# Kernel optimization log

Hardware: AMD Instinct MI355X
Metric: run time of the kernel (lower is better)

Reference implementation:

```python
import jax, jax.numpy as jnp
import numpy as np
from jax import lax

SEQ_LEN = 8192
TAGS = 2048

def setup_inputs() -> dict:
    key = jax.random.key(0)
    k1, k2, k3, k4, k5 = jax.random.split(key, 5)
    feats = jax.random.normal(k1, (SEQ_LEN, TAGS), dtype=jnp.float32)
    tags = jax.random.randint(k2, (SEQ_LEN,), 0, TAGS, dtype=jnp.int32)
    # nn.Parameter(torch.rand(...)) -> uniform [0,1)
    transitions = jax.random.uniform(k3, (TAGS, TAGS), dtype=jnp.float32)
    transitions_start = jax.random.uniform(k4, (TAGS,), dtype=jnp.float32)
    transitions_stop = jax.random.uniform(k5, (TAGS,), dtype=jnp.float32)
    return {
        "feats": feats,
        "transitions": transitions,
        "transitions_start": transitions_start,
        "transitions_stop": transitions_stop,
        "tags": tags,
    }

def reference(feats, transitions, transitions_start, transitions_stop, tags):
    # Linear-chain CRF negative log-likelihood.
    # transitions[next, prev] = score of transitioning prev -> next.
    L = feats.shape[0]

    # ---- forward (partition) score via log-sum-exp recurrence ----
    fv0 = transitions_start + feats[0]  # [T]

    def step(fv, feat):
        # new[j] = logsumexp_i(fv[i] + transitions[j, i]) + feat[j]
        nfv = jax.nn.logsumexp(fv[None, :] + transitions, axis=1) + feat
        return nfv, None

    fv, _ = lax.scan(step, fv0, feats[1:])
    forward_score = jax.nn.logsumexp(fv + transitions_stop)

    # ---- gold path score ----
    gold = (
        transitions_start[tags[0]]
        + feats[0, tags[0]]
        + jnp.sum(transitions[tags[1:], tags[:-1]])
        + jnp.sum(feats[jnp.arange(1, L), tags[1:]])
        + transitions_stop[tags[-1]]
    )

    return forward_score - gold
```

## Files before the change

### kernel.cpp

```cpp
#include <hip/hip_runtime.h>

#define SEQ  8192
#define NT   2048
#define NBLK 256
#define NTHR 512
#define LOG2E 1.4426950408889634f
#define LN2   0.6931471805599453f

#define LOAD_AG(p)     __hip_atomic_load((p), __ATOMIC_RELAXED, __HIP_MEMORY_SCOPE_AGENT)
#define STORE_AG(p, v) __hip_atomic_store((p), (v), __ATOMIC_RELAXED, __HIP_MEMORY_SCOPE_AGENT)

__device__ unsigned int g_z[2][NT];
__device__ float g_gold;

__device__ __forceinline__ unsigned int f32_to_bf16(float f) {
    unsigned int u = __float_as_uint(f);
    return (u + 0x7FFFu + ((u >> 16) & 1u)) >> 16;
}

__global__ void crf_init(const float* __restrict__ feats,
                         const float* __restrict__ tstart) {
    int i = blockIdx.x * blockDim.x + threadIdx.x;
    if (i < NT) {
        float z0 = __builtin_exp2f((tstart[i] + feats[i]) * LOG2E);
        g_z[0][i] = f32_to_bf16(z0);
        g_z[1][i] = 0xFFFF0000u;
    }
}

__global__ void crf_gold(const float* __restrict__ feats,
                         const float* __restrict__ trans,
                         const float* __restrict__ tstart,
                         const float* __restrict__ tstop,
                         const int*   __restrict__ tags) {
    __shared__ float part[16];
    int tid = threadIdx.x;
    float acc = 0.f;
    for (int t = 1 + tid; t < SEQ; t += 1024) {
        int cur = tags[t], prev = tags[t - 1];
        acc += trans[(size_t)cur * NT + prev] + feats[(size_t)t * NT + cur];
    }
    #pragma unroll
    for (int m = 1; m < 64; m <<= 1) acc += __shfl_xor(acc, m, 64);
    if ((tid & 63) == 0) part[tid >> 6] = acc;
    __syncthreads();
    if (tid == 0) {
        float S = 0.f;
        #pragma unroll
        for (int w = 0; w < 16; ++w) S += part[w];
        int t0 = tags[0], tl = tags[SEQ - 1];
        g_gold = S + tstart[t0] + feats[t0] + tstop[tl];
    }
}

__global__ void __launch_bounds__(NTHR)
crf_main(const float* __restrict__ feats, const float* __restrict__ trans,
         const float* __restrict__ tstop, float* __restrict__ out) {
    const int b   = blockIdx.x;
    const int tid = threadIdx.x;
    const int wv  = tid >> 6;
    const int l   = tid & 63;
    const int j   = b * 8 + wv;

    __shared__ float w_lds[2][NT];
    __shared__ float s_scale[2];
    __shared__ float red[8];

    float E[32];
    {
        const float* trow = trans + (size_t)j * NT;
        #pragma unroll
        for (int k = 0; k < 32; ++k)
            E[k] = __builtin_exp2f(trow[l + (k << 6)] * LOG2E);
    }

    float featv = feats[(size_t)NT + j];
    int esum = 0;

    for (int t = 1; t < SEQ; ++t) {
        const int par = (t - 1) & 1;
        const unsigned int need = (unsigned int)(t - 1);
        unsigned int* buf = g_z[par];

        #pragma unroll
        for (int q = 0; q < 4; ++q) {
            int i = tid + q * NTHR;
            unsigned int v;
            do { v = LOAD_AG(&buf[i]); } while ((v >> 16) != need);
            w_lds[par][i] = __uint_as_float(v << 16);
        }
        if (tid == 0) {
            unsigned int bits = __float_as_uint(w_lds[par][0]);
            int e = (int)((bits >> 23) & 0xFFu) - 127;
            s_scale[par] = __uint_as_float((unsigned int)(127 - e) << 23);
            esum += e;
        }
        float featnext = (t + 1 < SEQ) ? feats[(size_t)(t + 1) * NT + j] : 0.f;
        __syncthreads();

        float acc = 0.f;
        #pragma unroll
        for (int k = 0; k < 32; ++k)
            acc = fmaf(E[k], w_lds[par][l + (k << 6)], acc);
        #pragma unroll
        for (int m = 1; m < 64; m <<= 1) acc += __shfl_xor(acc, m, 64);

        if (l == 0) {
            float znew = acc * s_scale[par] * __builtin_exp2f(featv * LOG2E);
            STORE_AG(&g_z[t & 1][j],
                     ((unsigned int)t << 16) | f32_to_bf16(znew));
        }
        featv = featnext;
    }

    if (b == 0) {
        const unsigned int need = SEQ - 1;
        unsigned int* buf = g_z[(SEQ - 1) & 1];
        float acc = 0.f;
        #pragma unroll
        for (int q = 0; q < 4; ++q) {
            int i = tid + q * NTHR;
            unsigned int v;
            do { v = LOAD_AG(&buf[i]); } while ((v >> 16) != need);
            float w = __uint_as_float(v << 16);
            acc += w * __builtin_exp2f(tstop[i] * LOG2E);
        }
        #pragma unroll
        for (int m = 1; m < 64; m <<= 1) acc += __shfl_xor(acc, m, 64);
        if (l == 0) red[wv] = acc;
        __syncthreads();
        if (tid == 0) {
            float S = 0.f;
            #pragma unroll
            for (int w = 0; w < 8; ++w) S += red[w];
            float fwd = (__builtin_log2f(S) + (float)esum) * LN2;
            out[0] = fwd - g_gold;
        }
    }
}

extern "C" void kernel_launch(void* const* d_in, const int* in_sizes, int n_in,
                              void* d_out, int out_size, void* d_ws, size_t ws_size,
                              hipStream_t stream) {
    const float* feats  = (const float*)d_in[0];
    const float* trans  = (const float*)d_in[1];
    const float* tstart = (const float*)d_in[2];
    const float* tstop  = (const float*)d_in[3];
    const int*   tags   = (const int*)d_in[4];
    float* out = (float*)d_out;

    hipLaunchKernelGGL(crf_init, dim3(2), dim3(1024), 0, stream, feats, tstart);
    hipLaunchKernelGGL(crf_gold, dim3(1), dim3(1024), 0, stream,
                       feats, trans, tstart, tstop, tags);
    hipLaunchKernelGGL(crf_main, dim3(NBLK), dim3(NTHR), 0, stream,
                       feats, trans, tstop, out);
}
```

Before: 22.30 ms.

## Poll z vector with 64-bit atomic loads using 128 blocks of 1024 threads

Halves the number of persistent blocks and doubles the threads per block, so each thread polls a single 64-bit word holding two tagged bf16 values instead of four separate 32-bit words. This cuts per-step polling loads and the number of blocks contending on the global handoff each step. The exp of the next feature value is also computed ahead of the barrier. In exchange, 1024-thread blocks with 32 register-resident exp(transition) values per thread may raise register pressure, and each block's barrier now covers twice as many waves.

```diff
diff --git a/kernel.cpp b/kernel.cpp
--- a/kernel.cpp
+++ b/kernel.cpp
@@ -2,15 +2,15 @@
 
 #define SEQ  8192
 #define NT   2048
-#define NBLK 256
-#define NTHR 512
+#define NBLK 128
+#define NTHR 1024
 #define LOG2E 1.4426950408889634f
 #define LN2   0.6931471805599453f
 
-#define LOAD_AG(p)     __hip_atomic_load((p), __ATOMIC_RELAXED, __HIP_MEMORY_SCOPE_AGENT)
+#define LOAD_AG64(p)   __hip_atomic_load((p), __ATOMIC_RELAXED, __HIP_MEMORY_SCOPE_AGENT)
 #define STORE_AG(p, v) __hip_atomic_store((p), (v), __ATOMIC_RELAXED, __HIP_MEMORY_SCOPE_AGENT)
 
-__device__ unsigned int g_z[2][NT];
+__device__ __align__(16) unsigned int g_z[2][NT];
 __device__ float g_gold;
 
 __device__ __forceinline__ unsigned int f32_to_bf16(float f) {
@@ -60,11 +60,11 @@
     const int tid = threadIdx.x;
     const int wv  = tid >> 6;
     const int l   = tid & 63;
-    const int j   = b * 8 + wv;
+    const int j   = b * 16 + wv;
 
     __shared__ float w_lds[2][NT];
     __shared__ float s_scale[2];
-    __shared__ float red[8];
+    __shared__ float red[16];
 
     float E[32];
     {
@@ -74,28 +74,30 @@
             E[k] = __builtin_exp2f(trow[l + (k << 6)] * LOG2E);
     }
 
-    float featv = feats[(size_t)NT + j];
+    float fexp = __builtin_exp2f(feats[(size_t)NT + j] * LOG2E);
     int esum = 0;
 
     for (int t = 1; t < SEQ; ++t) {
         const int par = (t - 1) & 1;
         const unsigned int need = (unsigned int)(t - 1);
-        unsigned int* buf = g_z[par];
+        unsigned long long* buf64 = (unsigned long long*)g_z[par];
 
-        #pragma unroll
-        for (int q = 0; q < 4; ++q) {
-            int i = tid + q * NTHR;
-            unsigned int v;
-            do { v = LOAD_AG(&buf[i]); } while ((v >> 16) != need);
-            w_lds[par][i] = __uint_as_float(v << 16);
-        }
+        const unsigned long long want =
+            ((unsigned long long)need << 48) | ((unsigned long long)need << 16);
+        unsigned long long v;
+        do { v = LOAD_AG64(&buf64[tid]); }
+        while ((v & 0xFFFF0000FFFF0000ull) != want);
+
+        w_lds[par][2 * tid]     = __uint_as_float((unsigned int)(v & 0xFFFFu) << 16);
+        w_lds[par][2 * tid + 1] = __uint_as_float((unsigned int)((v >> 32) & 0xFFFFu) << 16);
+
         if (tid == 0) {
-            unsigned int bits = __float_as_uint(w_lds[par][0]);
-            int e = (int)((bits >> 23) & 0xFFu) - 127;
+            int e = (int)(((v >> 7) & 0xFFu)) - 127;
             s_scale[par] = __uint_as_float((unsigned int)(127 - e) << 23);
             esum += e;
         }
-        float featnext = (t + 1 < SEQ) ? feats[(size_t)(t + 1) * NT + j] : 0.f;
+        float fexpnext = (t + 1 < SEQ)
+            ? __builtin_exp2f(feats[(size_t)(t + 1) * NT + j] * LOG2E) : 0.f;
         __syncthreads();
 
         float acc = 0.f;
@@ -106,25 +108,26 @@
         for (int m = 1; m < 64; m <<= 1) acc += __shfl_xor(acc, m, 64);
 
         if (l == 0) {
-            float znew = acc * s_scale[par] * __builtin_exp2f(featv * LOG2E);
+            float znew = acc * s_scale[par] * fexp;
             STORE_AG(&g_z[t & 1][j],
                      ((unsigned int)t << 16) | f32_to_bf16(znew));
         }
-        featv = featnext;
+        fexp = fexpnext;
     }
 
     if (b == 0) {
         const unsigned int need = SEQ - 1;
-        unsigned int* buf = g_z[(SEQ - 1) & 1];
-        float acc = 0.f;
-        #pragma unroll
-        for (int q = 0; q < 4; ++q) {
-            int i = tid + q * NTHR;
-            unsigned int v;
-            do { v = LOAD_AG(&buf[i]); } while ((v >> 16) != need);
-            float w = __uint_as_float(v << 16);
-            acc += w * __builtin_exp2f(tstop[i] * LOG2E);
-        }
+        unsigned long long* buf64 = (unsigned long long*)g_z[(SEQ - 1) & 1];
+        const unsigned long long want =
+            ((unsigned long long)need << 48) | ((unsigned long long)need << 16);
+        unsigned long long v;
+        do { v = LOAD_AG64(&buf64[tid]); }
+        while ((v & 0xFFFF0000FFFF0000ull) != want);
+
+        float w0 = __uint_as_float((unsigned int)(v & 0xFFFFu) << 16);
+        float w1 = __uint_as_float((unsigned int)((v >> 32) & 0xFFFFu) << 16);
+        float acc = w0 * __builtin_exp2f(tstop[2 * tid] * LOG2E)
+                  + w1 * __builtin_exp2f(tstop[2 * tid + 1] * LOG2E);
         #pragma unroll
         for (int m = 1; m < 64; m <<= 1) acc += __shfl_xor(acc, m, 64);
         if (l == 0) red[wv] = acc;
@@ -132,7 +135,7 @@
         if (tid == 0) {
             float S = 0.f;
             #pragma unroll
-            for (int w = 0; w < 8; ++w) S += red[w];
+            for (int w = 0; w < 16; ++w) S += red[w];
             float fwd = (__builtin_log2f(S) + (float)esum) * LN2;
             out[0] = fwd - g_gold;
         }
```

Measured after the change: 41.54 ms. +86.3%, slower.
